# Kernel tuning notes

Measured on AMD Instinct MI355X. Metric: run time of the kernel, lower is better.

The kernel has to match this reference:

```python
import jax, jax.numpy as jnp
import numpy as np

NEG_INF = -1e30  # stand-in for float('-inf') masked_fill (safe for softmax)


def setup_inputs() -> dict:
    key = jax.random.key(0)
    ks = jax.random.split(key, 7)
    B, T, C, H, D = 4, 2048, 64, 6, 64
    s = 1.0 / np.sqrt(C)
    return {
        "x": jax.random.normal(ks[0], (B, T, C), dtype=jnp.float32),
        "y": jax.random.normal(ks[1], (B, T, C), dtype=jnp.float32),
        "Wq": jax.random.normal(ks[2], (H, C, D), dtype=jnp.float32) * s,
        "Wk": jax.random.normal(ks[3], (H, C, D), dtype=jnp.float32) * s,
        "Wv": jax.random.normal(ks[4], (H, C, D), dtype=jnp.float32) * s,
        "W_proj": jax.random.normal(ks[5], (H * D, C), dtype=jnp.float32) * (1.0 / np.sqrt(H * D)),
        "b_proj": jnp.zeros((C,), dtype=jnp.float32),
    }


def reference(x, y, Wq, Wk, Wv, W_proj, b_proj):
    # x, y: [B, T, C]; per-head projections stacked over H (heads vectorized).
    B, T, C = x.shape
    H, _, D = Wq.shape
    q = jnp.einsum("btc,hcd->bhtd", x, Wq)   # query from decoder input x
    k = jnp.einsum("btc,hcd->bhtd", y, Wk)   # key from encoder output y
    v = jnp.einsum("btc,hcd->bhtd", y, Wv)
    scale = D ** (-0.5)
    wei = jnp.einsum("bhtd,bhsd->bhts", q, k) * scale  # [B,H,T,T]
    # triu(ones(T,T), diagonal=1) future mask (causal)
    future = jnp.triu(jnp.ones((T, T), dtype=bool), k=1)
    wei = jnp.where(future, NEG_INF, wei)
    wei = jax.nn.softmax(wei, axis=-1)  # dropout = identity in eval
    out = jnp.einsum("bhts,bhsd->bhtd", wei, v)          # [B,H,T,D]
    out = out.transpose(0, 2, 1, 3).reshape(B, T, H * D)  # concat heads
    return out @ W_proj + b_proj                          # [B,T,C]
```

## Files before the change

kernel.cpp:

```cpp
#include <hip/hip_runtime.h>


typedef unsigned short u16t;
typedef __attribute__((ext_vector_type(8))) short short8;
typedef __attribute__((ext_vector_type(4))) float float4v;

#define MFMA16(a, b, c) __builtin_amdgcn_mfma_f32_16x16x32_bf16((a), (b), (c), 0, 0, 0)

union U8 { short8 s; unsigned u[4]; };

__device__ __forceinline__ float fexp2(float x) {
  return __builtin_amdgcn_exp2f(x);
}
__device__ __forceinline__ float bf2f(u16t u) {
  return __uint_as_float(((unsigned)u) << 16);
}
__device__ __forceinline__ u16t f2bf(float f) {
  unsigned u = __float_as_uint(f);
  u += 0x7fffu + ((u >> 16) & 1u);
  return (u16t)(u >> 16);
}
__device__ __forceinline__ unsigned bftr(float f) {
  return __float_as_uint(f) >> 16;
}
__device__ __forceinline__ short8 load8_f32_bf16(const float* p) {
  float4 f0 = *(const float4*)p;
  float4 f1 = *(const float4*)(p + 4);
  short8 r;
  r[0] = (short)f2bf(f0.x); r[1] = (short)f2bf(f0.y);
  r[2] = (short)f2bf(f0.z); r[3] = (short)f2bf(f0.w);
  r[4] = (short)f2bf(f1.x); r[5] = (short)f2bf(f1.y);
  r[6] = (short)f2bf(f1.z); r[7] = (short)f2bf(f1.w);
  return r;
}

constexpr int Bb = 4, Tt = 2048, Cc = 64, Hh = 6, Dd = 64;
constexpr int BH = Bb * Hh;
constexpr int NQT = Tt / 64;
constexpr int LDT = 72;
constexpr int LDV = 136;
constexpr int OST = 65;
#define QSCALE (0.125f * 1.44269504088896f)

__global__ __launch_bounds__(256) void prep_kernel(
    const float* __restrict__ Wq, const float* __restrict__ Wk,
    const float* __restrict__ Wv, const float* __restrict__ Wp,
    u16t* __restrict__ Wqt, u16t* __restrict__ Wkt,
    u16t* __restrict__ Wvt, u16t* __restrict__ Wpt) {
  int idx = blockIdx.x * 256 + threadIdx.x;
  {
    int h = idx >> 12, dc = idx & 4095, d = dc >> 6, c = dc & 63;
    int src = h * 4096 + c * 64 + d;
    Wqt[idx] = f2bf(Wq[src]);
    Wkt[idx] = f2bf(Wk[src]);
    Wvt[idx] = f2bf(Wv[src]);
  }
  {
    int c = idx / 384, r = idx - c * 384;
    Wpt[idx] = f2bf(Wp[r * 64 + c]);
  }
}

__global__ __launch_bounds__(256) void qkv_kernel(
    const float* __restrict__ x, const float* __restrict__ y,
    const u16t* __restrict__ Wqt, const u16t* __restrict__ Wkt,
    const u16t* __restrict__ Wvt,
    u16t* __restrict__ Q, u16t* __restrict__ K, u16t* __restrict__ Vt) {
  __shared__ __align__(16) u16t wtq[64 * LDT];
  __shared__ __align__(16) u16t wtk[64 * LDT];
  __shared__ __align__(16) u16t wtv[64 * LDT];

  int bid = blockIdx.x;
  int bh = bid >> 5, tt = bid & 31;
  int b = bh / Hh, h = bh - b * Hh;
  int tid = threadIdx.x;
  int w = tid >> 6, lane = tid & 63;
  int l15 = lane & 15, q4 = lane >> 4;

  {
    const u16t* wq = Wqt + h * 4096;
    const u16t* wk = Wkt + h * 4096;
    const u16t* wv = Wvt + h * 4096;
#pragma unroll
    for (int i = 0; i < 2; ++i) {
      int id = tid * 2 + i;
      int row = id >> 3, c8 = id & 7;
      *(uint4*)&wtq[row * LDT + c8 * 8] = *(const uint4*)(wq + id * 8);
      *(uint4*)&wtk[row * LDT + c8 * 8] = *(const uint4*)(wk + id * 8);
      *(uint4*)&wtv[row * LDT + c8 * 8] = *(const uint4*)(wv + id * 8);
    }
  }

  int trow = tt * 64 + w * 16 + l15;
  const float* xrow = x + ((size_t)b * Tt + trow) * Cc;
  const float* yrow = y + ((size_t)b * Tt + trow) * Cc;
  short8 xa[2], ya[2];
#pragma unroll
  for (int kc = 0; kc < 2; ++kc) {
    xa[kc] = load8_f32_bf16(xrow + kc * 32 + q4 * 8);
    ya[kc] = load8_f32_bf16(yrow + kc * 32 + q4 * 8);
  }
  __syncthreads();

  float4v qa4[4], ka4[4], va4[4];
#pragma unroll
  for (int nc = 0; nc < 4; ++nc) {
    qa4[nc] = (float4v){0.f, 0.f, 0.f, 0.f};
    ka4[nc] = (float4v){0.f, 0.f, 0.f, 0.f};
    va4[nc] = (float4v){0.f, 0.f, 0.f, 0.f};
  }
#pragma unroll
  for (int nc = 0; nc < 4; ++nc) {
#pragma unroll
    for (int kc = 0; kc < 2; ++kc) {
      int off = (nc * 16 + l15) * LDT + kc * 32 + q4 * 8;
      short8 bq = *(const short8*)&wtq[off];
      short8 bk = *(const short8*)&wtk[off];
      short8 bv = *(const short8*)&wtv[off];
      qa4[nc] = MFMA16(xa[kc], bq, qa4[nc]);
      ka4[nc] = MFMA16(ya[kc], bk, ka4[nc]);
      va4[nc] = MFMA16(ya[kc], bv, va4[nc]);
    }
  }
  __syncthreads();

#pragma unroll
  for (int reg = 0; reg < 4; ++reg) {
    int rloc = w * 16 + q4 * 4 + reg;
#pragma unroll
    for (int nc = 0; nc < 4; ++nc) {
      wtq[rloc * LDT + nc * 16 + l15] = f2bf(qa4[nc][reg] * QSCALE);
      wtk[rloc * LDT + nc * 16 + l15] = f2bf(ka4[nc][reg]);
      wtv[(nc * 16 + l15) * LDT + rloc] = f2bf(va4[nc][reg]);
    }
  }
  __syncthreads();

  size_t tilebase = ((size_t)bh * Tt + tt * 64) * Dd;
#pragma unroll
  for (int i = 0; i < 2; ++i) {
    int id = tid * 2 + i;
    int row = id >> 3, c8 = id & 7;
    *(uint4*)&Q[tilebase + row * 64 + c8 * 8] = *(const uint4*)&wtq[row * LDT + c8 * 8];
    *(uint4*)&K[tilebase + row * 64 + c8 * 8] = *(const uint4*)&wtk[row * LDT + c8 * 8];
    *(uint4*)&Vt[((size_t)bh * 64 + row) * Tt + tt * 64 + c8 * 8] =
        *(const uint4*)&wtv[row * LDT + c8 * 8];
  }
}

__global__ __launch_bounds__(256) void attn_kernel(
    const u16t* __restrict__ Q, const u16t* __restrict__ K,
    const u16t* __restrict__ Vt, u16t* __restrict__ att) {
  __shared__ __align__(16) unsigned char smem[128 * LDT * 2 + 64 * LDV * 2];
  u16t* Kl = (u16t*)smem;
  u16t* Vl = (u16t*)(smem + 128 * LDT * 2);
  float* Ol = (float*)smem;
  float* Ll = (float*)(smem + 64 * OST * 4);

  int bid = blockIdx.x;
  int bh = bid % BH;
  int qt = (NQT - 1) - bid / BH;
  int b = bh / Hh, h = bh - (bh / Hh) * Hh;
  int tid = threadIdx.x;
  int w = tid >> 6;
  int lane = tid & 63;
  int l15 = lane & 15, q4 = lane >> 4;

  short8 qf[4][2];
#pragma unroll
  for (int it = 0; it < 4; ++it) {
    const u16t* qb = Q + ((size_t)bh * Tt + qt * 64 + it * 16 + l15) * Dd;
    qf[it][0] = *(const short8*)(qb + q4 * 8);
    qf[it][1] = *(const short8*)(qb + 32 + q4 * 8);
  }

  float4v O[4][4];
#pragma unroll
  for (int it = 0; it < 4; ++it)
#pragma unroll
    for (int nc = 0; nc < 4; ++nc) O[it][nc] = (float4v){0.f, 0.f, 0.f, 0.f};
  float l_[4] = {0.f, 0.f, 0.f, 0.f};

  const u16t* Kbh = K + (size_t)bh * Tt * Dd;
  const u16t* Vbh = Vt + (size_t)bh * Dd * Tt;
  const int bsmax = qt >> 1;

  for (int bs = 0; bs <= bsmax; ++bs) {
    __syncthreads();
    {
      const u16t* ks = Kbh + (size_t)bs * 128 * 64;
      const u16t* vs = Vbh + bs * 128;
#pragma unroll
      for (int i = 0; i < 4; ++i) {
        int id = tid + i * 256;
        *(uint4*)&Kl[(id >> 3) * LDT + (id & 7) * 8] =
            *(const uint4*)(ks + (size_t)(id >> 3) * 64 + (id & 7) * 8);
        *(uint4*)&Vl[(id >> 4) * LDV + (id & 15) * 8] =
            *(const uint4*)(vs + (size_t)(id >> 4) * Tt + (id & 15) * 8);
      }
    }
    __syncthreads();

    bool d0 = (2 * bs == qt);
    bool s1 = (2 * bs + 1 > qt);
    bool d1 = (2 * bs + 1 == qt);

    short8 kf00 = *(const short8*)&Kl[(w * 16 + l15) * LDT + q4 * 8];
    short8 kf01 = *(const short8*)&Kl[(w * 16 + l15) * LDT + 32 + q4 * 8];
    short8 kf10 = kf00, kf11 = kf01;
    if (!s1) {
      kf10 = *(const short8*)&Kl[(64 + w * 16 + l15) * LDT + q4 * 8];
      kf11 = *(const short8*)&Kl[(64 + w * 16 + l15) * LDT + 32 + q4 * 8];
    }
    short8 vf[4];
#pragma unroll
    for (int nc = 0; nc < 4; ++nc) {
      U8 t;
      *(uint2*)&t.u[0] = *(const uint2*)&Vl[(nc * 16 + l15) * LDV + w * 16 + q4 * 4];
      *(uint2*)&t.u[2] = *(const uint2*)&Vl[(nc * 16 + l15) * LDV + 64 + w * 16 + q4 * 4];
      vf[nc] = t.s;
    }

#pragma unroll
    for (int it = 0; it < 4; ++it) {
      if (d0 && w > it) continue;
      float4v S0 = (float4v){0.f, 0.f, 0.f, 0.f};
      S0 = MFMA16(kf00, qf[it][0], S0);
      S0 = MFMA16(kf01, qf[it][1], S0);
      bool m0 = d0 && (w == it);
      float p0[4], p1[4];
#pragma unroll
      for (int reg = 0; reg < 4; ++reg) {
        p0[reg] = (m0 && (q4 * 4 + reg) > l15) ? 0.f : fexp2(S0[reg]);
        l_[it] += p0[reg];
      }
      if (s1 || (d1 && w > it)) {
#pragma unroll
        for (int reg = 0; reg < 4; ++reg) p1[reg] = 0.f;
      } else {
        float4v S1 = (float4v){0.f, 0.f, 0.f, 0.f};
        S1 = MFMA16(kf10, qf[it][0], S1);
        S1 = MFMA16(kf11, qf[it][1], S1);
        bool m1 = d1 && (w == it);
#pragma unroll
        for (int reg = 0; reg < 4; ++reg) {
          p1[reg] = (m1 && (q4 * 4 + reg) > l15) ? 0.f : fexp2(S1[reg]);
          l_[it] += p1[reg];
        }
      }
      U8 pa;
      pa.u[0] = bftr(p0[0]) | (bftr(p0[1]) << 16);
      pa.u[1] = bftr(p0[2]) | (bftr(p0[3]) << 16);
      pa.u[2] = bftr(p1[0]) | (bftr(p1[1]) << 16);
      pa.u[3] = bftr(p1[2]) | (bftr(p1[3]) << 16);
#pragma unroll
      for (int nc = 0; nc < 4; ++nc)
        O[it][nc] = MFMA16(pa.s, vf[nc], O[it][nc]);
    }
  }

#pragma unroll
  for (int it = 0; it < 4; ++it) {
    l_[it] += __shfl_xor(l_[it], 16);
    l_[it] += __shfl_xor(l_[it], 32);
  }

  __syncthreads();
#pragma unroll
  for (int r = 0; r < 4; ++r) {
#pragma unroll
    for (int itc = 0; itc < 4; ++itc) {
      if (((itc - w) & 3) == r) {
#pragma unroll
        for (int nc = 0; nc < 4; ++nc)
#pragma unroll
          for (int reg = 0; reg < 4; ++reg) {
            int addr = (itc * 16 + q4 * 4 + reg) * OST + nc * 16 + l15;
            if (r == 0) Ol[addr] = O[itc][nc][reg];
            else        Ol[addr] += O[itc][nc][reg];
          }
        if (q4 == 0) {
          if (r == 0) Ll[itc * 16 + l15] = l_[itc];
          else        Ll[itc * 16 + l15] += l_[itc];
        }
      }
    }
    __syncthreads();
  }

#pragma unroll
  for (int i = 0; i < 2; ++i) {
    int id = tid * 2 + i;
    int row = id >> 3, c8 = id & 7;
    float inv = 1.0f / Ll[row];
    const float* orow = &Ol[row * OST + c8 * 8];
    U8 o;
#pragma unroll
    for (int k = 0; k < 4; ++k)
      o.u[k] = f2bf(orow[2 * k] * inv) | ((unsigned)f2bf(orow[2 * k + 1] * inv) << 16);
    int t = qt * 64 + row;
    *(uint4*)&att[((size_t)b * Tt + t) * (Hh * Dd) + h * Dd + c8 * 8] = *(const uint4*)&o;
  }
}

constexpr int LDP = 392;

__global__ __launch_bounds__(256) void proj_kernel(
    const u16t* __restrict__ att, const u16t* __restrict__ Wpt,
    const float* __restrict__ bp, float* __restrict__ out) {
  __shared__ __align__(16) u16t wpt[64 * LDP];

  int bid = blockIdx.x;
  int tid = threadIdx.x;
  int w = tid >> 6, lane = tid & 63;
  int l15 = lane & 15, q4 = lane >> 4;

#pragma unroll
  for (int i = 0; i < 12; ++i) {
    int id = tid + i * 256;
    int r = id / 48, c8 = id - r * 48;
    *(uint4*)&wpt[r * LDP + c8 * 8] = *(const uint4*)(Wpt + id * 8);
  }
  __syncthreads();

  int row0 = bid * 64 + w * 16;
  const u16t* arow = att + (size_t)(row0 + l15) * 384;

  float4v acc[4];
#pragma unroll
  for (int nc = 0; nc < 4; ++nc) acc[nc] = (float4v){0.f, 0.f, 0.f, 0.f};

#pragma unroll
  for (int kc = 0; kc < 12; ++kc) {
    short8 a = *(const short8*)(arow + kc * 32 + q4 * 8);
#pragma unroll
    for (int nc = 0; nc < 4; ++nc) {
      short8 bfr = *(const short8*)&wpt[(nc * 16 + l15) * LDP + kc * 32 + q4 * 8];
      acc[nc] = MFMA16(a, bfr, acc[nc]);
    }
  }

  float bv[4];
#pragma unroll
  for (int nc = 0; nc < 4; ++nc) bv[nc] = bp[nc * 16 + l15];
#pragma unroll
  for (int reg = 0; reg < 4; ++reg) {
    int t = row0 + q4 * 4 + reg;
    size_t obase = (size_t)t * 64;
#pragma unroll
    for (int nc = 0; nc < 4; ++nc)
      out[obase + nc * 16 + l15] = acc[nc][reg] + bv[nc];
  }
}

extern "C" void kernel_launch(void* const* d_in, const int* in_sizes, int n_in,
                              void* d_out, int out_size, void* d_ws, size_t ws_size,
                              hipStream_t stream) {
  const float* x  = (const float*)d_in[0];
  const float* y  = (const float*)d_in[1];
  const float* Wq = (const float*)d_in[2];
  const float* Wk = (const float*)d_in[3];
  const float* Wv = (const float*)d_in[4];
  const float* Wp = (const float*)d_in[5];
  const float* bp = (const float*)d_in[6];
  float* out = (float*)d_out;

  const size_t NBH = (size_t)BH * Tt * Dd;
  u16t* Qs   = (u16t*)d_ws;
  u16t* Ks   = Qs + NBH;
  u16t* Vts  = Ks + NBH;
  u16t* attb = Vts + NBH;
  u16t* Wqt  = attb + NBH;
  u16t* Wkt  = Wqt + 24576;
  u16t* Wvt  = Wkt + 24576;
  u16t* Wpt  = Wvt + 24576;

  prep_kernel<<<96, 256, 0, stream>>>(Wq, Wk, Wv, Wp, Wqt, Wkt, Wvt, Wpt);
  qkv_kernel<<<BH * NQT, 256, 0, stream>>>(x, y, Wqt, Wkt, Wvt, Qs, Ks, Vts);
  attn_kernel<<<BH * NQT, 256, 0, stream>>>(Qs, Ks, Vts, attb);
  proj_kernel<<<(Bb * Tt) / 64, 256, 0, stream>>>(attb, Wpt, bp, out);
}
```

Baseline: 119.5 us.

## Split long causal query tiles across two KV chunks with merge kernel

Query tiles in the upper half of the sequence now have their key/value range split into two halves handled by separate blocks. Each block writes unnormalized partial outputs and row sums to a global scratch buffer, and a new merge kernel adds them and normalizes into bf16. The goal is to balance the causal workload and raise block count to shorten the tail. It adds extra global traffic for partials and an additional kernel launch.

New measurement: 137.6 us. 15.2% more time.

```diff
diff --git a/kernel.cpp b/kernel.cpp
--- a/kernel.cpp
+++ b/kernel.cpp
@@ -39,7 +39,9 @@
 constexpr int NQT = Tt / 64;
 constexpr int LDT = 72;
 constexpr int LDV = 136;
-constexpr int OST = 65;
+constexpr int OST = 68;
+constexpr int RPB = 48;
+constexpr int PSLOT = 64 * 64 + 64;
 #define QSCALE (0.125f * 1.44269504088896f)
 
 __global__ __launch_bounds__(256) void prep_kernel(
@@ -150,7 +152,8 @@
 
 __global__ __launch_bounds__(256) void attn_kernel(
     const u16t* __restrict__ Q, const u16t* __restrict__ K,
-    const u16t* __restrict__ Vt, u16t* __restrict__ att) {
+    const u16t* __restrict__ Vt, u16t* __restrict__ att,
+    float* __restrict__ pbuf) {
   __shared__ __align__(16) unsigned char smem[128 * LDT * 2 + 64 * LDV * 2];
   u16t* Kl = (u16t*)smem;
   u16t* Vl = (u16t*)(smem + 128 * LDT * 2);
@@ -158,14 +161,22 @@
   float* Ll = (float*)(smem + 64 * OST * 4);
 
   int bid = blockIdx.x;
-  int bh = bid % BH;
-  int qt = (NQT - 1) - bid / BH;
+  int bh = bid / RPB, r = bid - bh * RPB;
+  int qt, jc;
+  if (r < 32) { qt = 16 + (r >> 1); jc = r & 1; }
+  else        { qt = 47 - r;        jc = 0;     }
   int b = bh / Hh, h = bh - (bh / Hh) * Hh;
   int tid = threadIdx.x;
   int w = tid >> 6;
   int lane = tid & 63;
   int l15 = lane & 15, q4 = lane >> 4;
 
+  const int bsmax = qt >> 1;
+  const int nslab = bsmax + 1;
+  const int c0 = (nslab + 1) >> 1;
+  int bs0 = 0, bs1 = nslab;
+  if (qt >= 16) { bs0 = jc ? c0 : 0; bs1 = jc ? nslab : c0; }
+
   short8 qf[4][2];
 #pragma unroll
   for (int it = 0; it < 4; ++it) {
@@ -183,9 +194,8 @@
 
   const u16t* Kbh = K + (size_t)bh * Tt * Dd;
   const u16t* Vbh = Vt + (size_t)bh * Dd * Tt;
-  const int bsmax = qt >> 1;
-
-  for (int bs = 0; bs <= bsmax; ++bs) {
+
+  for (int bs = bs0; bs < bs1; ++bs) {
     __syncthreads();
     {
       const u16t* ks = Kbh + (size_t)bs * 128 * 64;
@@ -267,40 +277,80 @@
 
   __syncthreads();
 #pragma unroll
-  for (int r = 0; r < 4; ++r) {
+  for (int rr = 0; rr < 4; ++rr) {
 #pragma unroll
     for (int itc = 0; itc < 4; ++itc) {
-      if (((itc - w) & 3) == r) {
+      if (((itc - w) & 3) == rr) {
 #pragma unroll
         for (int nc = 0; nc < 4; ++nc)
 #pragma unroll
           for (int reg = 0; reg < 4; ++reg) {
             int addr = (itc * 16 + q4 * 4 + reg) * OST + nc * 16 + l15;
-            if (r == 0) Ol[addr] = O[itc][nc][reg];
-            else        Ol[addr] += O[itc][nc][reg];
+            if (rr == 0) Ol[addr] = O[itc][nc][reg];
+            else         Ol[addr] += O[itc][nc][reg];
           }
         if (q4 == 0) {
-          if (r == 0) Ll[itc * 16 + l15] = l_[itc];
-          else        Ll[itc * 16 + l15] += l_[itc];
+          if (rr == 0) Ll[itc * 16 + l15] = l_[itc];
+          else         Ll[itc * 16 + l15] += l_[itc];
         }
       }
     }
     __syncthreads();
   }
 
-#pragma unroll
-  for (int i = 0; i < 2; ++i) {
-    int id = tid * 2 + i;
-    int row = id >> 3, c8 = id & 7;
-    float inv = 1.0f / Ll[row];
-    const float* orow = &Ol[row * OST + c8 * 8];
-    U8 o;
-#pragma unroll
-    for (int k = 0; k < 4; ++k)
-      o.u[k] = f2bf(orow[2 * k] * inv) | ((unsigned)f2bf(orow[2 * k + 1] * inv) << 16);
-    int t = qt * 64 + row;
-    *(uint4*)&att[((size_t)b * Tt + t) * (Hh * Dd) + h * Dd + c8 * 8] = *(const uint4*)&o;
-  }
+  if (qt < 16) {
+#pragma unroll
+    for (int i = 0; i < 2; ++i) {
+      int id = tid * 2 + i;
+      int row = id >> 3, c8 = id & 7;
+      float inv = 1.0f / Ll[row];
+      const float* orow = &Ol[row * OST + c8 * 8];
+      U8 o;
+#pragma unroll
+      for (int k = 0; k < 4; ++k)
+        o.u[k] = f2bf(orow[2 * k] * inv) | ((unsigned)f2bf(orow[2 * k + 1] * inv) << 16);
+      int t = qt * 64 + row;
+      *(uint4*)&att[((size_t)b * Tt + t) * (Hh * Dd) + h * Dd + c8 * 8] = *(const uint4*)&o;
+    }
+  } else {
+    float* ps = pbuf + (size_t)(bh * 32 + (qt - 16) * 2 + jc) * PSLOT;
+    int row = tid >> 2, seg = tid & 3;
+#pragma unroll
+    for (int k = 0; k < 4; ++k) {
+      float4 v = *(const float4*)&Ol[row * OST + seg * 16 + k * 4];
+      *(float4*)&ps[row * 64 + seg * 16 + k * 4] = v;
+    }
+    if (tid < 64) ps[4096 + tid] = Ll[tid];
+  }
+}
+
+__global__ __launch_bounds__(256) void merge_kernel(
+    const float* __restrict__ pbuf, u16t* __restrict__ att) {
+  int bid = blockIdx.x;
+  int bh = bid >> 4, qtl = bid & 15;
+  int b = bh / Hh, h = bh - b * Hh;
+  int tid = threadIdx.x;
+  int row = tid >> 2, seg = tid & 3;
+
+  const float* p0 = pbuf + (size_t)(bh * 32 + qtl * 2) * PSLOT;
+  const float* p1 = p0 + PSLOT;
+  float inv = 1.0f / (p0[4096 + row] + p1[4096 + row]);
+
+  U8 o[2];
+#pragma unroll
+  for (int half = 0; half < 2; ++half) {
+#pragma unroll
+    for (int k = 0; k < 2; ++k) {
+      float4 a = *(const float4*)&p0[row * 64 + seg * 16 + half * 8 + k * 4];
+      float4 c = *(const float4*)&p1[row * 64 + seg * 16 + half * 8 + k * 4];
+      o[half].u[k * 2 + 0] = f2bf((a.x + c.x) * inv) | ((unsigned)f2bf((a.y + c.y) * inv) << 16);
+      o[half].u[k * 2 + 1] = f2bf((a.z + c.z) * inv) | ((unsigned)f2bf((a.w + c.w) * inv) << 16);
+    }
+  }
+  int t = (16 + qtl) * 64 + row;
+  u16t* dst = att + ((size_t)b * Tt + t) * (Hh * Dd) + h * Dd + seg * 16;
+  *(uint4*)dst = *(const uint4*)&o[0];
+  *(uint4*)(dst + 8) = *(const uint4*)&o[1];
 }
 
 constexpr int LDP = 392;
@@ -374,9 +424,11 @@
   u16t* Wkt  = Wqt + 24576;
   u16t* Wvt  = Wkt + 24576;
   u16t* Wpt  = Wvt + 24576;
+  float* pbuf = (float*)(Wpt + 24576);
 
   prep_kernel<<<96, 256, 0, stream>>>(Wq, Wk, Wv, Wp, Wqt, Wkt, Wvt, Wpt);
   qkv_kernel<<<BH * NQT, 256, 0, stream>>>(x, y, Wqt, Wkt, Wvt, Qs, Ks, Vts);
-  attn_kernel<<<BH * NQT, 256, 0, stream>>>(Qs, Ks, Vts, attb);
+  attn_kernel<<<BH * RPB, 256, 0, stream>>>(Qs, Ks, Vts, attb, pbuf);
+  merge_kernel<<<BH * 16, 256, 0, stream>>>(pbuf, attb);
   proj_kernel<<<(Bb * Tt) / 64, 256, 0, stream>>>(attb, Wpt, bp, out);
 }
```

## Double-buffer 64-key K/V tiles with register prefetch in attention loop

Applied to the files above, without the earlier changes.

The attention loop now walks 64-key tiles instead of 128-key tiles. Each next K/V tile is loaded into registers during the current tile's compute and written into a second LDS buffer afterwards, so there is one barrier per iteration and global latency overlaps the MFMA work. The cost is that the P·V MFMA now runs with half of its 32-wide reduction zero-padded, which doubles the P·V MFMA issue per key. There are also twice as many loop iterations and barriers. The output staging padding and LDS aliasing are adjusted to fit the new buffers.

After: 151.7 us. 27.0% more time.

```diff
diff --git a/kernel.cpp b/kernel.cpp
--- a/kernel.cpp
+++ b/kernel.cpp
@@ -38,8 +38,7 @@
 constexpr int BH = Bb * Hh;
 constexpr int NQT = Tt / 64;
 constexpr int LDT = 72;
-constexpr int LDV = 136;
-constexpr int OST = 65;
+constexpr int OST = 68;
 #define QSCALE (0.125f * 1.44269504088896f)
 
 __global__ __launch_bounds__(256) void prep_kernel(
@@ -151,11 +150,10 @@
 __global__ __launch_bounds__(256) void attn_kernel(
     const u16t* __restrict__ Q, const u16t* __restrict__ K,
     const u16t* __restrict__ Vt, u16t* __restrict__ att) {
-  __shared__ __align__(16) unsigned char smem[128 * LDT * 2 + 64 * LDV * 2];
-  u16t* Kl = (u16t*)smem;
-  u16t* Vl = (u16t*)(smem + 128 * LDT * 2);
-  float* Ol = (float*)smem;
-  float* Ll = (float*)(smem + 64 * OST * 4);
+  __shared__ __align__(16) u16t Kb[2][64 * LDT];
+  __shared__ __align__(16) u16t Vb[2][64 * LDT];
+  float* Ol = (float*)&Kb[0][0];
+  float* Ll = (float*)&Vb[0][0];
 
   int bid = blockIdx.x;
   int bh = bid % BH;
@@ -183,80 +181,81 @@
 
   const u16t* Kbh = K + (size_t)bh * Tt * Dd;
   const u16t* Vbh = Vt + (size_t)bh * Dd * Tt;
-  const int bsmax = qt >> 1;
-
-  for (int bs = 0; bs <= bsmax; ++bs) {
-    __syncthreads();
-    {
-      const u16t* ks = Kbh + (size_t)bs * 128 * 64;
-      const u16t* vs = Vbh + bs * 128;
-#pragma unroll
-      for (int i = 0; i < 4; ++i) {
-        int id = tid + i * 256;
-        *(uint4*)&Kl[(id >> 3) * LDT + (id & 7) * 8] =
-            *(const uint4*)(ks + (size_t)(id >> 3) * 64 + (id & 7) * 8);
-        *(uint4*)&Vl[(id >> 4) * LDV + (id & 15) * 8] =
-            *(const uint4*)(vs + (size_t)(id >> 4) * Tt + (id & 15) * 8);
+
+  uint4 lk[2], lv[2];
+#pragma unroll
+  for (int i = 0; i < 2; ++i) {
+    int id = tid * 2 + i;
+    lk[i] = *(const uint4*)(Kbh + (id >> 3) * 64 + (id & 7) * 8);
+    lv[i] = *(const uint4*)(Vbh + (size_t)(id >> 3) * Tt + (id & 7) * 8);
+  }
+#pragma unroll
+  for (int i = 0; i < 2; ++i) {
+    int id = tid * 2 + i;
+    *(uint4*)&Kb[0][(id >> 3) * LDT + (id & 7) * 8] = lk[i];
+    *(uint4*)&Vb[0][(id >> 3) * LDT + (id & 7) * 8] = lv[i];
+  }
+  __syncthreads();
+
+  for (int bs = 0; bs <= qt; ++bs) {
+    int cur = bs & 1;
+    if (bs < qt) {
+      const u16t* ks = Kbh + (size_t)(bs + 1) * 4096;
+      const u16t* vs = Vbh + (bs + 1) * 64;
+#pragma unroll
+      for (int i = 0; i < 2; ++i) {
+        int id = tid * 2 + i;
+        lk[i] = *(const uint4*)(ks + (id >> 3) * 64 + (id & 7) * 8);
+        lv[i] = *(const uint4*)(vs + (size_t)(id >> 3) * Tt + (id & 7) * 8);
       }
     }
-    __syncthreads();
-
-    bool d0 = (2 * bs == qt);
-    bool s1 = (2 * bs + 1 > qt);
-    bool d1 = (2 * bs + 1 == qt);
-
-    short8 kf00 = *(const short8*)&Kl[(w * 16 + l15) * LDT + q4 * 8];
-    short8 kf01 = *(const short8*)&Kl[(w * 16 + l15) * LDT + 32 + q4 * 8];
-    short8 kf10 = kf00, kf11 = kf01;
-    if (!s1) {
-      kf10 = *(const short8*)&Kl[(64 + w * 16 + l15) * LDT + q4 * 8];
-      kf11 = *(const short8*)&Kl[(64 + w * 16 + l15) * LDT + 32 + q4 * 8];
-    }
+
+    const u16t* Kc = &Kb[cur][0];
+    const u16t* Vc = &Vb[cur][0];
+
+    short8 kf0 = *(const short8*)&Kc[(w * 16 + l15) * LDT + q4 * 8];
+    short8 kf1 = *(const short8*)&Kc[(w * 16 + l15) * LDT + 32 + q4 * 8];
     short8 vf[4];
 #pragma unroll
     for (int nc = 0; nc < 4; ++nc) {
+      uint2 vv = *(const uint2*)&Vc[(nc * 16 + l15) * LDT + w * 16 + q4 * 4];
       U8 t;
-      *(uint2*)&t.u[0] = *(const uint2*)&Vl[(nc * 16 + l15) * LDV + w * 16 + q4 * 4];
-      *(uint2*)&t.u[2] = *(const uint2*)&Vl[(nc * 16 + l15) * LDV + 64 + w * 16 + q4 * 4];
+      t.u[0] = vv.x; t.u[1] = vv.y; t.u[2] = 0u; t.u[3] = 0u;
       vf[nc] = t.s;
     }
 
+    bool diag = (bs == qt);
 #pragma unroll
     for (int it = 0; it < 4; ++it) {
-      if (d0 && w > it) continue;
-      float4v S0 = (float4v){0.f, 0.f, 0.f, 0.f};
-      S0 = MFMA16(kf00, qf[it][0], S0);
-      S0 = MFMA16(kf01, qf[it][1], S0);
-      bool m0 = d0 && (w == it);
-      float p0[4], p1[4];
+      if (diag && w > it) continue;
+      float4v S = (float4v){0.f, 0.f, 0.f, 0.f};
+      S = MFMA16(kf0, qf[it][0], S);
+      S = MFMA16(kf1, qf[it][1], S);
+      float p[4];
 #pragma unroll
       for (int reg = 0; reg < 4; ++reg) {
-        p0[reg] = (m0 && (q4 * 4 + reg) > l15) ? 0.f : fexp2(S0[reg]);
-        l_[it] += p0[reg];
-      }
-      if (s1 || (d1 && w > it)) {
-#pragma unroll
-        for (int reg = 0; reg < 4; ++reg) p1[reg] = 0.f;
-      } else {
-        float4v S1 = (float4v){0.f, 0.f, 0.f, 0.f};
-        S1 = MFMA16(kf10, qf[it][0], S1);
-        S1 = MFMA16(kf11, qf[it][1], S1);
-        bool m1 = d1 && (w == it);
-#pragma unroll
-        for (int reg = 0; reg < 4; ++reg) {
-          p1[reg] = (m1 && (q4 * 4 + reg) > l15) ? 0.f : fexp2(S1[reg]);
-          l_[it] += p1[reg];
-        }
+        p[reg] = (diag && w == it && (q4 * 4 + reg) > l15) ? 0.f : fexp2(S[reg]);
+        l_[it] += p[reg];
       }
       U8 pa;
-      pa.u[0] = bftr(p0[0]) | (bftr(p0[1]) << 16);
-      pa.u[1] = bftr(p0[2]) | (bftr(p0[3]) << 16);
-      pa.u[2] = bftr(p1[0]) | (bftr(p1[1]) << 16);
-      pa.u[3] = bftr(p1[2]) | (bftr(p1[3]) << 16);
+      pa.u[0] = bftr(p[0]) | (bftr(p[1]) << 16);
+      pa.u[1] = bftr(p[2]) | (bftr(p[3]) << 16);
+      pa.u[2] = 0u; pa.u[3] = 0u;
 #pragma unroll
       for (int nc = 0; nc < 4; ++nc)
         O[it][nc] = MFMA16(pa.s, vf[nc], O[it][nc]);
     }
+
+    if (bs < qt) {
+      int nxt = cur ^ 1;
+#pragma unroll
+      for (int i = 0; i < 2; ++i) {
+        int id = tid * 2 + i;
+        *(uint4*)&Kb[nxt][(id >> 3) * LDT + (id & 7) * 8] = lk[i];
+        *(uint4*)&Vb[nxt][(id >> 3) * LDT + (id & 7) * 8] = lv[i];
+      }
+    }
+    __syncthreads();
   }
 
 #pragma unroll
@@ -265,23 +264,22 @@
     l_[it] += __shfl_xor(l_[it], 32);
   }
 
-  __syncthreads();
-#pragma unroll
-  for (int r = 0; r < 4; ++r) {
+#pragma unroll
+  for (int rr = 0; rr < 4; ++rr) {
 #pragma unroll
     for (int itc = 0; itc < 4; ++itc) {
-      if (((itc - w) & 3) == r) {
+      if (((itc - w) & 3) == rr) {
 #pragma unroll
         for (int nc = 0; nc < 4; ++nc)
 #pragma unroll
           for (int reg = 0; reg < 4; ++reg) {
             int addr = (itc * 16 + q4 * 4 + reg) * OST + nc * 16 + l15;
-            if (r == 0) Ol[addr] = O[itc][nc][reg];
-            else        Ol[addr] += O[itc][nc][reg];
+            if (rr == 0) Ol[addr] = O[itc][nc][reg];
+            else         Ol[addr] += O[itc][nc][reg];
           }
         if (q4 == 0) {
-          if (r == 0) Ll[itc * 16 + l15] = l_[itc];
-          else        Ll[itc * 16 + l15] += l_[itc];
+          if (rr == 0) Ll[itc * 16 + l15] = l_[itc];
+          else         Ll[itc * 16 + l15] += l_[itc];
         }
       }
     }
```
